# Performance work log

Hardware: AMD Instinct MI355X
Metric: run time of the kernel (lower is better)

Reference implementation:

```python
import jax, jax.numpy as jnp
import numpy as np

N = 50000      # num_nodes
R = 8          # num_relations
FIN = 128      # in_channels
H = 128        # hidden_channels
E = 800000     # num_edges (avg degree 16)


def _xavier(key, shape):
    fan_in, fan_out = shape[-2], shape[-1]
    lim = np.sqrt(6.0 / (fan_in + fan_out)).astype(np.float32)
    return jax.random.uniform(key, shape, jnp.float32, -lim, lim)


def setup_inputs() -> dict:
    key = jax.random.key(0)
    ks = jax.random.split(key, 10)
    return {
        "x": jax.random.normal(ks[0], (N, FIN), jnp.float32),
        "edge_index": jax.random.randint(ks[1], (2, E), 0, N, jnp.int32),
        "edge_type": jax.random.randint(ks[2], (E,), 0, R, jnp.int32),
        "rel_w0": _xavier(ks[3], (R, FIN, H)),
        "root_w0": _xavier(ks[4], (FIN, H)),
        "bias0": jnp.zeros((H,), jnp.float32),
        "rel_w1": _xavier(ks[5], (R, H, H)),
        "root_w1": _xavier(ks[6], (H, H)),
        "bias1": jnp.zeros((H,), jnp.float32),
        "rel_emb": _xavier(ks[7], (R, H)),
    }


def _rgcn_conv(x, src, dst, etype, rel_w, root_w, bias):
    # RGCNConv (PyG, aggr='mean'): out_i = root(x_i) + sum_r W_r * mean_{j in N_r(i)} x_j
    n = x.shape[0]
    seg = dst * R + etype                                   # fused (node, relation) segment id
    msgs = x[src]                                           # [E, F] gather
    sums = jax.ops.segment_sum(msgs, seg, num_segments=n * R)
    cnt = jax.ops.segment_sum(jnp.ones((src.shape[0], 1), x.dtype), seg, num_segments=n * R)
    mean = (sums / jnp.maximum(cnt, 1.0)).reshape(n, R, -1)  # [N, R, F]
    return jnp.einsum('nrf,rfh->nh', mean, rel_w) + x @ root_w + bias


def reference(x, edge_index, edge_type, rel_w0, root_w0, bias0,
              rel_w1, root_w1, bias1, rel_emb):
    src, dst = edge_index[0], edge_index[1]
    h = _rgcn_conv(x, src, dst, edge_type, rel_w0, root_w0, bias0)
    h = jax.nn.relu(h)  # dropout in eval mode (identity)
    h = _rgcn_conv(h, src, dst, edge_type, rel_w1, root_w1, bias1)
    return (h, rel_emb)
```

## Files before the change

kernel.cpp:

```cpp
#include <hip/hip_runtime.h>

typedef unsigned short ushort_t;
typedef __attribute__((ext_vector_type(8))) short short8;
typedef __attribute__((ext_vector_type(4))) float f32x4;
typedef __attribute__((ext_vector_type(4))) int int4v;

#define RNUM 8
#define FDIM 128
#define KDIM 1152

__device__ __forceinline__ float bf2f(ushort_t u) {
    union { unsigned int i; float f; } x;
    x.i = ((unsigned int)u) << 16;
    return x.f;
}
__device__ __forceinline__ ushort_t f2bf(float f) {
    union { float f; unsigned int i; } x;
    x.f = f;
    unsigned int u = x.i;
    u += 0x7fffu + ((u >> 16) & 1u);
    return (ushort_t)(u >> 16);
}

__device__ __forceinline__ void gl_lds16(const void* g, void* s) {
    __builtin_amdgcn_global_load_lds(
        (const __attribute__((address_space(1))) unsigned int*)g,
        (__attribute__((address_space(3))) unsigned int*)s, 16, 0, 0);
}


__global__ void init_head(int* __restrict__ head, int n) {
    int i = blockIdx.x * 256 + threadIdx.x;
    if (i < n) head[i] = -1;
}

__global__ void link_kernel(const int* __restrict__ dst, const int* __restrict__ et,
                            int* head, int* __restrict__ nxt, int E) {
    int i = blockIdx.x * 256 + threadIdx.x;
    if (i < E) {
        int seg = dst[i] * RNUM + et[i];
        nxt[i] = atomicExch(&head[seg], i);
    }
}


__global__ __launch_bounds__(256) void transpose_w(const float* __restrict__ rel_w,
                                                   const float* __restrict__ root_w,
                                                   ushort_t* __restrict__ Wt) {
    int r = blockIdx.x;
    const float* src = (r < 8) ? (rel_w + r * 16384) : root_w;
    __shared__ ushort_t t[128 * 130];
    for (int idx = threadIdx.x; idx < 16384; idx += 256)
        t[(idx >> 7) * 130 + (idx & 127)] = f2bf(src[idx]);
    __syncthreads();
    ushort_t* d = Wt + r * 16384;
    for (int idx = threadIdx.x; idx < 16384; idx += 256)
        d[idx] = t[(idx & 127) * 130 + (idx >> 7)];
}


__global__ void cast_x(const float* __restrict__ x, ushort_t* __restrict__ Mx, int total) {
    int i = (blockIdx.x * 256 + threadIdx.x) * 8;
    if (i >= total) return;
    float4 v0 = *(const float4*)(x + i);
    float4 v1 = *(const float4*)(x + i + 4);
    ushort_t o[8] = {f2bf(v0.x), f2bf(v0.y), f2bf(v0.z), f2bf(v0.w),
                     f2bf(v1.x), f2bf(v1.y), f2bf(v1.z), f2bf(v1.w)};
    int row = i >> 7, col = i & 127;
    *(int4v*)(Mx + (size_t)row * KDIM + 1024 + col) = *(int4v*)o;
}


__global__ __launch_bounds__(256) void seg_mean(const int* __restrict__ head,
                                                const int* __restrict__ nxt,
                                                const int* __restrict__ esrc,
                                                ushort_t* Mx, int NSEG) {
    int t = blockIdx.x * 256 + threadIdx.x;
    int seg = t >> 4;
    int l16 = t & 15;
    if (seg >= NSEG) return;
    float acc[8];
#pragma unroll
    for (int k = 0; k < 8; ++k) acc[k] = 0.f;
    const ushort_t* gbase = Mx + 1024 + (size_t)l16 * 8;
    int cnt = 0;
    int j = head[seg];
    while (j >= 0) {
        int s = esrc[j];
        int jn = nxt[j];
        int4v v = *(const int4v*)(gbase + (size_t)s * KDIM);
        ushort_t* p = (ushort_t*)&v;
#pragma unroll
        for (int k = 0; k < 8; ++k) acc[k] += bf2f(p[k]);
        ++cnt;
        j = jn;
    }
    float sc = (cnt > 0) ? 1.0f / (float)cnt : 0.f;
    ushort_t ov[8];
#pragma unroll
    for (int k = 0; k < 8; ++k) ov[k] = f2bf(acc[k] * sc);
    *(int4v*)(Mx + (size_t)(seg >> 3) * KDIM + (seg & 7) * 128 + l16 * 8) = *(int4v*)ov;
}


template <bool FINAL>
__global__ __launch_bounds__(256) void rgcn_gemm(
    const ushort_t* Mx, const ushort_t* __restrict__ Wt,
    const float* __restrict__ bias, float* __restrict__ outF,
    ushort_t* MxOut, int N) {
    __shared__ ushort_t As[128 * 128];
    __shared__ ushort_t Bs[128 * 128];
    int tid = threadIdx.x;
    int wid = tid >> 6, lane = tid & 63;
    int l16 = lane & 15, q = lane >> 4;
    int nodeBase = blockIdx.x * 128;

    f32x4 acc[2][8];
#pragma unroll
    for (int rt = 0; rt < 2; ++rt)
#pragma unroll
        for (int ct = 0; ct < 8; ++ct) acc[rt][ct] = (f32x4){0.f, 0.f, 0.f, 0.f};

    for (int r = 0; r < 9; ++r) {
        __syncthreads();
#pragma unroll
        for (int i = 0; i < 8; ++i) {
            int L = i * 256 + tid;
            int row = L >> 4;
            int c = (L & 15) ^ (row & 15);
            gl_lds16(Mx + (size_t)(nodeBase + row) * KDIM + r * 128 + c * 8,
                     (char*)As + (size_t)L * 16);
            gl_lds16(Wt + r * 16384 + row * 128 + c * 8,
                     (char*)Bs + (size_t)L * 16);
        }
        __syncthreads();
#pragma unroll
        for (int s = 0; s < 4; ++s) {
            int pos = ((s * 4 + q) ^ l16) * 16;
            short8 a0 = *(const short8*)((const char*)As + ((2 * wid + 0) * 16 + l16) * 256 + pos);
            short8 a1 = *(const short8*)((const char*)As + ((2 * wid + 1) * 16 + l16) * 256 + pos);
#pragma unroll
            for (int ct = 0; ct < 8; ++ct) {
                short8 b = *(const short8*)((const char*)Bs + (ct * 16 + l16) * 256 + pos);
                acc[0][ct] = __builtin_amdgcn_mfma_f32_16x16x32_bf16(a0, b, acc[0][ct], 0, 0, 0);
                acc[1][ct] = __builtin_amdgcn_mfma_f32_16x16x32_bf16(a1, b, acc[1][ct], 0, 0, 0);
            }
        }
    }
#pragma unroll
    for (int rt = 0; rt < 2; ++rt) {
#pragma unroll
        for (int ct = 0; ct < 8; ++ct) {
            int h = ct * 16 + l16;
            float bv = bias[h];
#pragma unroll
            for (int reg = 0; reg < 4; ++reg) {
                int node = nodeBase + (2 * wid + rt) * 16 + q * 4 + reg;
                if (node < N) {
                    float v = acc[rt][ct][reg] + bv;
                    if (FINAL) {
                        outF[(size_t)node * FDIM + h] = v;
                    } else {
                        v = fmaxf(v, 0.f);
                        MxOut[(size_t)node * KDIM + 1024 + h] = f2bf(v);
                    }
                }
            }
        }
    }
}

__global__ void copy_emb(const float* __restrict__ e, float* __restrict__ out, int n) {
    int i = blockIdx.x * 256 + threadIdx.x;
    if (i < n) out[i] = e[i];
}


extern "C" void kernel_launch(void* const* d_in, const int* in_sizes, int n_in,
                              void* d_out, int out_size, void* d_ws, size_t ws_size,
                              hipStream_t stream) {
    const float* x        = (const float*)d_in[0];
    const int* edge_index = (const int*)d_in[1];
    const int* edge_type  = (const int*)d_in[2];
    const float* rel_w0   = (const float*)d_in[3];
    const float* root_w0  = (const float*)d_in[4];
    const float* bias0    = (const float*)d_in[5];
    const float* rel_w1   = (const float*)d_in[6];
    const float* root_w1  = (const float*)d_in[7];
    const float* bias1    = (const float*)d_in[8];
    const float* rel_emb  = (const float*)d_in[9];

    int N = in_sizes[0] / FDIM;
    int E = in_sizes[1] / 2;
    int NSEG = N * RNUM;
    const int* src = edge_index;
    const int* dst = edge_index + E;

    int nb_gemm = (N + 127) / 128;
    int NPAD = nb_gemm * 128;

    char* w = (char*)d_ws;
    auto alloc = [&](size_t bytes) -> char* {
        char* p = w;
        w += (bytes + 255) & ~(size_t)255;
        return p;
    };
    int* head    = (int*)alloc((size_t)NSEG * 4);
    int* nxt     = (int*)alloc((size_t)E * 4);
    ushort_t* Wt = (ushort_t*)alloc((size_t)2 * 9 * 16384 * 2);
    ushort_t* Mx = (ushort_t*)alloc((size_t)NPAD * KDIM * 2);
    (void)ws_size; (void)n_in; (void)out_size;

    int nb_seg  = (NSEG + 255) / 256;
    int nb_E    = (E + 255) / 256;
    int nb_mean = (NSEG * 16) / 256;
    int nb_cast = (N * FDIM) / (256 * 8);

    init_head<<<nb_seg, 256, 0, stream>>>(head, NSEG);
    link_kernel<<<nb_E, 256, 0, stream>>>(dst, edge_type, head, nxt, E);
    transpose_w<<<9, 256, 0, stream>>>(rel_w0, root_w0, Wt);
    transpose_w<<<9, 256, 0, stream>>>(rel_w1, root_w1, Wt + 9 * 16384);
    cast_x<<<nb_cast, 256, 0, stream>>>(x, Mx, N * FDIM);

    seg_mean<<<nb_mean, 256, 0, stream>>>(head, nxt, src, Mx, NSEG);
    rgcn_gemm<false><<<nb_gemm, 256, 0, stream>>>(Mx, Wt, bias0, nullptr, Mx, N);
    seg_mean<<<nb_mean, 256, 0, stream>>>(head, nxt, src, Mx, NSEG);
    rgcn_gemm<true><<<nb_gemm, 256, 0, stream>>>(Mx, Wt + 9 * 16384, bias1,
                                                 (float*)d_out, nullptr, N);
    copy_emb<<<4, 256, 0, stream>>>(rel_emb, (float*)d_out + (size_t)N * FDIM,
                                    in_sizes[9]);
}
```

Measured before the change: 335.9 us.

## Walk four segment linked lists per thread with next-edge prefetch in seg_mean

Each 16-lane group in seg_mean now handles four consecutive (node, relation) segments at once, so up to four independent pointer chases are in flight per thread. It also loads the next edge's source index and next pointer ahead of the feature gather, which shortens the dependent-load chain. The goal is to hide global-memory latency in the linked-list traversal. In exchange the grid has a quarter as many threads, the loop runs as long as the longest of the four lists, and register use grows.

```diff
diff --git a/kernel.cpp b/kernel.cpp
--- a/kernel.cpp
+++ b/kernel.cpp
@@ -76,30 +76,61 @@
                                                 const int* __restrict__ esrc,
                                                 ushort_t* Mx, int NSEG) {
     int t = blockIdx.x * 256 + threadIdx.x;
-    int seg = t >> 4;
+    int g = t >> 4;
     int l16 = t & 15;
-    if (seg >= NSEG) return;
-    float acc[8];
-#pragma unroll
-    for (int k = 0; k < 8; ++k) acc[k] = 0.f;
+    int segBase = g * 4;
+    if (segBase >= NSEG) return;
     const ushort_t* gbase = Mx + 1024 + (size_t)l16 * 8;
-    int cnt = 0;
-    int j = head[seg];
-    while (j >= 0) {
-        int s = esrc[j];
-        int jn = nxt[j];
-        int4v v = *(const int4v*)(gbase + (size_t)s * KDIM);
-        ushort_t* p = (ushort_t*)&v;
-#pragma unroll
-        for (int k = 0; k < 8; ++k) acc[k] += bf2f(p[k]);
-        ++cnt;
-        j = jn;
-    }
-    float sc = (cnt > 0) ? 1.0f / (float)cnt : 0.f;
-    ushort_t ov[8];
-#pragma unroll
-    for (int k = 0; k < 8; ++k) ov[k] = f2bf(acc[k] * sc);
-    *(int4v*)(Mx + (size_t)(seg >> 3) * KDIM + (seg & 7) * 128 + l16 * 8) = *(int4v*)ov;
+
+    float acc[4][8];
+    int cnt[4];
+    int j[4], s[4], nx[4];
+#pragma unroll
+    for (int c = 0; c < 4; ++c) {
+        cnt[c] = 0;
+#pragma unroll
+        for (int k = 0; k < 8; ++k) acc[c][k] = 0.f;
+        int sg = segBase + c;
+        j[c] = (sg < NSEG) ? head[sg] : -1;
+    }
+#pragma unroll
+    for (int c = 0; c < 4; ++c)
+        if (j[c] >= 0) { s[c] = esrc[j[c]]; nx[c] = nxt[j[c]]; }
+
+    while ((j[0] & j[1] & j[2] & j[3]) >= 0) {
+        int4v v[4];
+#pragma unroll
+        for (int c = 0; c < 4; ++c)
+            if (j[c] >= 0) v[c] = *(const int4v*)(gbase + (size_t)s[c] * KDIM);
+        int s2[4], nx2[4];
+#pragma unroll
+        for (int c = 0; c < 4; ++c)
+            if (j[c] >= 0 && nx[c] >= 0) { s2[c] = esrc[nx[c]]; nx2[c] = nxt[nx[c]]; }
+#pragma unroll
+        for (int c = 0; c < 4; ++c) {
+            if (j[c] >= 0) {
+                const ushort_t* p = (const ushort_t*)&v[c];
+#pragma unroll
+                for (int k = 0; k < 8; ++k) acc[c][k] += bf2f(p[k]);
+                ++cnt[c];
+                j[c] = nx[c];
+                s[c] = s2[c];
+                nx[c] = nx2[c];
+            }
+        }
+    }
+
+#pragma unroll
+    for (int c = 0; c < 4; ++c) {
+        int sg = segBase + c;
+        if (sg < NSEG) {
+            float sc = (cnt[c] > 0) ? 1.0f / (float)cnt[c] : 0.f;
+            ushort_t ov[8];
+#pragma unroll
+            for (int k = 0; k < 8; ++k) ov[k] = f2bf(acc[c][k] * sc);
+            *(int4v*)(Mx + (size_t)(sg >> 3) * KDIM + (sg & 7) * 128 + l16 * 8) = *(int4v*)ov;
+        }
+    }
 }
 
 
@@ -213,7 +244,8 @@
 
     int nb_seg  = (NSEG + 255) / 256;
     int nb_E    = (E + 255) / 256;
-    int nb_mean = (NSEG * 16) / 256;
+    int ngrp    = (NSEG + 3) / 4;
+    int nb_mean = (ngrp * 16 + 255) / 256;
     int nb_cast = (N * FDIM) / (256 * 8);
 
     init_head<<<nb_seg, 256, 0, stream>>>(head, NSEG);
```

Result: slower. 353.5 us (+5.2%).

## Split per-segment edge lists into four chains and pack src with next

Applied to the files above, without the earlier changes.

Each (node, relation) segment now gets four linked-list heads, picked by edge index mod 4, instead of one. The source id and next pointer are packed into one int2 record. seg_mean walks the four chains at the same time, issuing up to four independent row gathers per iteration, which shortens the dependent pointer-chasing latency chain. The cost is a head array four times larger to initialise and read, and more divergent control flow when chain lengths differ.

```diff
diff --git a/kernel.cpp b/kernel.cpp
--- a/kernel.cpp
+++ b/kernel.cpp
@@ -34,12 +34,14 @@
     if (i < n) head[i] = -1;
 }
 
-__global__ void link_kernel(const int* __restrict__ dst, const int* __restrict__ et,
-                            int* head, int* __restrict__ nxt, int E) {
+__global__ void link_kernel(const int* __restrict__ src, const int* __restrict__ dst,
+                            const int* __restrict__ et,
+                            int* head, int2* __restrict__ meta, int E) {
     int i = blockIdx.x * 256 + threadIdx.x;
     if (i < E) {
         int seg = dst[i] * RNUM + et[i];
-        nxt[i] = atomicExch(&head[seg], i);
+        int prev = atomicExch(&head[seg * 4 + (i & 3)], i);
+        meta[i] = make_int2(src[i], prev);
     }
 }
 
@@ -71,30 +73,51 @@
 }
 
 
-__global__ __launch_bounds__(256) void seg_mean(const int* __restrict__ head,
-                                                const int* __restrict__ nxt,
-                                                const int* __restrict__ esrc,
+__global__ __launch_bounds__(256) void seg_mean(const int4v* __restrict__ head4,
+                                                const int2* __restrict__ meta,
                                                 ushort_t* Mx, int NSEG) {
     int t = blockIdx.x * 256 + threadIdx.x;
     int seg = t >> 4;
     int l16 = t & 15;
     if (seg >= NSEG) return;
+    const ushort_t* gbase = Mx + 1024 + (size_t)l16 * 8;
+
     float acc[8];
 #pragma unroll
     for (int k = 0; k < 8; ++k) acc[k] = 0.f;
-    const ushort_t* gbase = Mx + 1024 + (size_t)l16 * 8;
+
+    int4v h4 = head4[seg];
+    int j[4], s[4], n[4];
+#pragma unroll
+    for (int c = 0; c < 4; ++c) j[c] = h4[c];
+#pragma unroll
+    for (int c = 0; c < 4; ++c)
+        if (j[c] >= 0) { int2 m = meta[j[c]]; s[c] = m.x; n[c] = m.y; }
+
     int cnt = 0;
-    int j = head[seg];
-    while (j >= 0) {
-        int s = esrc[j];
-        int jn = nxt[j];
-        int4v v = *(const int4v*)(gbase + (size_t)s * KDIM);
-        ushort_t* p = (ushort_t*)&v;
-#pragma unroll
-        for (int k = 0; k < 8; ++k) acc[k] += bf2f(p[k]);
-        ++cnt;
-        j = jn;
-    }
+    while ((j[0] & j[1] & j[2] & j[3]) >= 0) {
+        int4v v[4];
+#pragma unroll
+        for (int c = 0; c < 4; ++c)
+            if (j[c] >= 0) v[c] = *(const int4v*)(gbase + (size_t)s[c] * KDIM);
+        int2 m2[4];
+#pragma unroll
+        for (int c = 0; c < 4; ++c)
+            if (j[c] >= 0 && n[c] >= 0) m2[c] = meta[n[c]];
+#pragma unroll
+        for (int c = 0; c < 4; ++c) {
+            if (j[c] >= 0) {
+                const ushort_t* p = (const ushort_t*)&v[c];
+#pragma unroll
+                for (int k = 0; k < 8; ++k) acc[k] += bf2f(p[k]);
+                ++cnt;
+                j[c] = n[c];
+                s[c] = m2[c].x;
+                n[c] = m2[c].y;
+            }
+        }
+    }
+
     float sc = (cnt > 0) ? 1.0f / (float)cnt : 0.f;
     ushort_t ov[8];
 #pragma unroll
@@ -205,26 +228,26 @@
         w += (bytes + 255) & ~(size_t)255;
         return p;
     };
-    int* head    = (int*)alloc((size_t)NSEG * 4);
-    int* nxt     = (int*)alloc((size_t)E * 4);
+    int* head    = (int*)alloc((size_t)NSEG * 4 * 4);
+    int2* meta   = (int2*)alloc((size_t)E * 8);
     ushort_t* Wt = (ushort_t*)alloc((size_t)2 * 9 * 16384 * 2);
     ushort_t* Mx = (ushort_t*)alloc((size_t)NPAD * KDIM * 2);
     (void)ws_size; (void)n_in; (void)out_size;
 
-    int nb_seg  = (NSEG + 255) / 256;
+    int nb_head = (NSEG * 4 + 255) / 256;
     int nb_E    = (E + 255) / 256;
     int nb_mean = (NSEG * 16) / 256;
     int nb_cast = (N * FDIM) / (256 * 8);
 
-    init_head<<<nb_seg, 256, 0, stream>>>(head, NSEG);
-    link_kernel<<<nb_E, 256, 0, stream>>>(dst, edge_type, head, nxt, E);
+    init_head<<<nb_head, 256, 0, stream>>>(head, NSEG * 4);
+    link_kernel<<<nb_E, 256, 0, stream>>>(src, dst, edge_type, head, meta, E);
     transpose_w<<<9, 256, 0, stream>>>(rel_w0, root_w0, Wt);
     transpose_w<<<9, 256, 0, stream>>>(rel_w1, root_w1, Wt + 9 * 16384);
     cast_x<<<nb_cast, 256, 0, stream>>>(x, Mx, N * FDIM);
 
-    seg_mean<<<nb_mean, 256, 0, stream>>>(head, nxt, src, Mx, NSEG);
+    seg_mean<<<nb_mean, 256, 0, stream>>>((const int4v*)head, meta, Mx, NSEG);
     rgcn_gemm<false><<<nb_gemm, 256, 0, stream>>>(Mx, Wt, bias0, nullptr, Mx, N);
-    seg_mean<<<nb_mean, 256, 0, stream>>>(head, nxt, src, Mx, NSEG);
+    seg_mean<<<nb_mean, 256, 0, stream>>>((const int4v*)head, meta, Mx, NSEG);
     rgcn_gemm<true><<<nb_gemm, 256, 0, stream>>>(Mx, Wt + 9 * 16384, bias1,
                                                  (float*)d_out, nullptr, N);
     copy_emb<<<4, 256, 0, stream>>>(rel_emb, (float*)d_out + (size_t)N * FDIM,
```

After: 323.9 us. 1.04x faster.
